# Performance work log

Measured on AMD Instinct MI355X. Metric: run time of the kernel, lower is better.

## Reference

```python
import jax, jax.numpy as jnp
import numpy as np

K_V = 0.5      # input voltage scaling
G_OFF = 1e-5   # off conductance (S)
G_ON = 1e-3    # on conductance (S)


def setup_inputs() -> dict:
    key = jax.random.key(0)
    k1, k2 = jax.random.split(key)
    batch, size_in, size_out = 256, 1024, 1024
    stdv = 1.0 / np.sqrt(size_in)
    x = jax.random.normal(k1, (batch, size_in), dtype=jnp.float32)
    weights = jax.random.normal(k2, (size_out, size_in), dtype=jnp.float32) * stdv
    bias = jnp.zeros((size_out,), dtype=jnp.float32)
    return {"x": x, "weights": weights, "bias": bias}


def reference(x, weights, bias):
    batch = x.shape[0]
    # append bias column of ones: inputs [batch, in+1]
    inputs = jnp.concatenate([x, jnp.ones((batch, 1), dtype=x.dtype)], axis=1)
    # weights_and_bias [in+1, out]
    wb = jnp.concatenate([weights.T, bias[None, :]], axis=0)
    V = K_V * inputs
    max_wb = jnp.max(jnp.abs(wb))
    k_G = (G_ON - G_OFF) / max_wb
    k_I = K_V * k_G
    G_eff = k_G * wb
    G_pos = G_OFF + jnp.maximum(G_eff, 0.0)
    G_neg = G_OFF - jnp.minimum(G_eff, 0.0)
    # interleave pos/neg columns -> G [in+1, 2*out]
    G = jnp.reshape(jnp.stack([G_pos, G_neg], axis=-1), (wb.shape[0], -1))
    # sum over input lines == matmul (avoids torch's [batch,in+1,2*out] intermediate)
    I = jnp.einsum('bi,io->bo', V, G)
    I_total = I[:, 0::2] - I[:, 1::2]
    return I_total / k_I
```

## Files before the change

kernel.cpp:

```cpp
#include <hip/hip_runtime.h>
#include <hip/hip_bf16.h>


typedef __attribute__((ext_vector_type(4))) float  f32x4;
typedef __attribute__((ext_vector_type(8))) short  bf16x8;

#define BATCH    256
#define SIZE_IN  1024
#define SIZE_OUT 1024

#define BM  64
#define BN  64
#define BK  64
#define LDK 72
#define NT  (SIZE_IN / BK)

__global__ __launch_bounds__(256)
void memristor_gemm(const float* __restrict__ X, const float* __restrict__ W,
                    const float* __restrict__ bias, float* __restrict__ out) {
    __shared__ alignas(16) ushort Alds[2][BM][LDK];
    __shared__ alignas(16) ushort Blds[2][BN][LDK];

    const int t    = threadIdx.x;
    const int lr   = t >> 4;
    const int lc   = (t & 15) << 2;
    const int brow = blockIdx.y * BM;
    const int bcol = blockIdx.x * BN;

    const int wid  = t >> 6;
    const int lane = t & 63;
    const int wr   = wid >> 1;
    const int wc   = wid & 1;
    const int fr   = lane & 15;
    const int fg   = lane >> 4;

    const float* Aptr = X + (size_t)(brow + lr) * SIZE_IN + lc;
    const float* Bptr = W + (size_t)(bcol + lr) * SIZE_IN + lc;

    f32x4 ar[4], br[4];

    auto stage = [&](int buf) {
        #pragma unroll
        for (int q = 0; q < 4; ++q) {
            union { struct { __hip_bfloat162 a, b; } h; uint2 u; } pa, pb;
            float2 f0; f0.x = ar[q].x; f0.y = ar[q].y;
            float2 f1; f1.x = ar[q].z; f1.y = ar[q].w;
            pa.h.a = __float22bfloat162_rn(f0);
            pa.h.b = __float22bfloat162_rn(f1);
            float2 g0; g0.x = br[q].x; g0.y = br[q].y;
            float2 g1; g1.x = br[q].z; g1.y = br[q].w;
            pb.h.a = __float22bfloat162_rn(g0);
            pb.h.b = __float22bfloat162_rn(g1);
            *(uint2*)&Alds[buf][lr + q * 16][lc] = pa.u;
            *(uint2*)&Blds[buf][lr + q * 16][lc] = pb.u;
        }
    };

    #pragma unroll
    for (int q = 0; q < 4; ++q) {
        ar[q] = *(const f32x4*)(Aptr + q * 16 * SIZE_IN);
        br[q] = *(const f32x4*)(Bptr + q * 16 * SIZE_IN);
    }
    stage(0);
    __syncthreads();

    const f32x4 zero = {0.f, 0.f, 0.f, 0.f};
    f32x4 acc[2][2] = {{zero, zero}, {zero, zero}};

    int cur = 0;
    for (int kt = 0; kt < NT; ++kt) {
        const bool pf = (kt + 1 < NT);
        if (pf) {
            const int k = (kt + 1) * BK;
            #pragma unroll
            for (int q = 0; q < 4; ++q) {
                ar[q] = *(const f32x4*)(Aptr + q * 16 * SIZE_IN + k);
                br[q] = *(const f32x4*)(Bptr + q * 16 * SIZE_IN + k);
            }
        }
        #pragma unroll
        for (int kk = 0; kk < 2; ++kk) {
            bf16x8 af[2], bfv[2];
            #pragma unroll
            for (int m = 0; m < 2; ++m)
                af[m] = *(const bf16x8*)&Alds[cur][wr * 32 + m * 16 + fr][kk * 32 + fg * 8];
            #pragma unroll
            for (int n = 0; n < 2; ++n)
                bfv[n] = *(const bf16x8*)&Blds[cur][wc * 32 + n * 16 + fr][kk * 32 + fg * 8];
            #pragma unroll
            for (int m = 0; m < 2; ++m)
                #pragma unroll
                for (int n = 0; n < 2; ++n)
                    acc[m][n] = __builtin_amdgcn_mfma_f32_16x16x32_bf16(
                        af[m], bfv[n], acc[m][n], 0, 0, 0);
        }
        if (pf) stage(cur ^ 1);
        __syncthreads();
        cur ^= 1;
    }

    #pragma unroll
    for (int n = 0; n < 2; ++n) {
        const int col = bcol + wc * 32 + n * 16 + fr;
        const float bv = bias[col];
        #pragma unroll
        for (int m = 0; m < 2; ++m) {
            const int row0 = brow + wr * 32 + m * 16 + fg * 4;
            #pragma unroll
            for (int j = 0; j < 4; ++j) {
                out[(size_t)(row0 + j) * SIZE_OUT + col] = acc[m][n][j] + bv;
            }
        }
    }
}

extern "C" void kernel_launch(void* const* d_in, const int* in_sizes, int n_in,
                              void* d_out, int out_size, void* d_ws, size_t ws_size,
                              hipStream_t stream) {
    const float* x  = (const float*)d_in[0];
    const float* w  = (const float*)d_in[1];
    const float* b  = (const float*)d_in[2];
    float* out      = (float*)d_out;

    dim3 grid(SIZE_OUT / BN, BATCH / BM);
    dim3 block(256);
    hipLaunchKernelGGL(memristor_gemm, grid, block, 0, stream, x, w, b, out);
}
```

Measured before the change: 73.02 us.

## Replace LDS-staged GEMM with register-direct MFMA loads and split-K reduction

```diff
diff --git a/kernel.cpp b/kernel.cpp
--- a/kernel.cpp
+++ b/kernel.cpp
@@ -9,108 +9,58 @@
 #define SIZE_IN  1024
 #define SIZE_OUT 1024
 
-#define BM  64
-#define BN  64
-#define BK  64
-#define LDK 72
-#define NT  (SIZE_IN / BK)
+static __device__ inline bf16x8 pack8(f32x4 lo, f32x4 hi) {
+    union { struct { __hip_bfloat162 a, b, c, d; } h; bf16x8 v; } u;
+    float2 f;
+    f.x = lo.x; f.y = lo.y; u.h.a = __float22bfloat162_rn(f);
+    f.x = lo.z; f.y = lo.w; u.h.b = __float22bfloat162_rn(f);
+    f.x = hi.x; f.y = hi.y; u.h.c = __float22bfloat162_rn(f);
+    f.x = hi.z; f.y = hi.w; u.h.d = __float22bfloat162_rn(f);
+    return u.v;
+}
 
-__global__ __launch_bounds__(256)
+__global__ __launch_bounds__(512, 2)
 void memristor_gemm(const float* __restrict__ X, const float* __restrict__ W,
                     const float* __restrict__ bias, float* __restrict__ out) {
-    __shared__ alignas(16) ushort Alds[2][BM][LDK];
-    __shared__ alignas(16) ushort Blds[2][BN][LDK];
+    __shared__ f32x4 red[4][64];
 
     const int t    = threadIdx.x;
-    const int lr   = t >> 4;
-    const int lc   = (t & 15) << 2;
-    const int brow = blockIdx.y * BM;
-    const int bcol = blockIdx.x * BN;
-
+    const int lane = t & 63;
     const int wid  = t >> 6;
-    const int lane = t & 63;
-    const int wr   = wid >> 1;
-    const int wc   = wid & 1;
+    const int ks   = wid >> 2;
+    const int wq   = wid & 3;
+    const int wr   = wq >> 1;
+    const int wc   = wq & 1;
     const int fr   = lane & 15;
     const int fg   = lane >> 4;
 
-    const float* Aptr = X + (size_t)(brow + lr) * SIZE_IN + lc;
-    const float* Bptr = W + (size_t)(bcol + lr) * SIZE_IN + lc;
+    const int brow = blockIdx.y * 32;
+    const int bcol = blockIdx.x * 32;
 
-    f32x4 ar[4], br[4];
+    const float* Ap = X + (size_t)(brow + wr * 16 + fr) * SIZE_IN + ks * 512 + fg * 8;
+    const float* Bp = W + (size_t)(bcol + wc * 16 + fr) * SIZE_IN + ks * 512 + fg * 8;
 
-    auto stage = [&](int buf) {
-        #pragma unroll
-        for (int q = 0; q < 4; ++q) {
-            union { struct { __hip_bfloat162 a, b; } h; uint2 u; } pa, pb;
-            float2 f0; f0.x = ar[q].x; f0.y = ar[q].y;
-            float2 f1; f1.x = ar[q].z; f1.y = ar[q].w;
-            pa.h.a = __float22bfloat162_rn(f0);
-            pa.h.b = __float22bfloat162_rn(f1);
-            float2 g0; g0.x = br[q].x; g0.y = br[q].y;
-            float2 g1; g1.x = br[q].z; g1.y = br[q].w;
-            pb.h.a = __float22bfloat162_rn(g0);
-            pb.h.b = __float22bfloat162_rn(g1);
-            *(uint2*)&Alds[buf][lr + q * 16][lc] = pa.u;
-            *(uint2*)&Blds[buf][lr + q * 16][lc] = pb.u;
-        }
-    };
-
+    f32x4 acc = {0.f, 0.f, 0.f, 0.f};
     #pragma unroll
-    for (int q = 0; q < 4; ++q) {
-        ar[q] = *(const f32x4*)(Aptr + q * 16 * SIZE_IN);
-        br[q] = *(const f32x4*)(Bptr + q * 16 * SIZE_IN);
-    }
-    stage(0);
-    __syncthreads();
-
-    const f32x4 zero = {0.f, 0.f, 0.f, 0.f};
-    f32x4 acc[2][2] = {{zero, zero}, {zero, zero}};
-
-    int cur = 0;
-    for (int kt = 0; kt < NT; ++kt) {
-        const bool pf = (kt + 1 < NT);
-        if (pf) {
-            const int k = (kt + 1) * BK;
-            #pragma unroll
-            for (int q = 0; q < 4; ++q) {
-                ar[q] = *(const f32x4*)(Aptr + q * 16 * SIZE_IN + k);
-                br[q] = *(const f32x4*)(Bptr + q * 16 * SIZE_IN + k);
-            }
-        }
-        #pragma unroll
-        for (int kk = 0; kk < 2; ++kk) {
-            bf16x8 af[2], bfv[2];
-            #pragma unroll
-            for (int m = 0; m < 2; ++m)
-                af[m] = *(const bf16x8*)&Alds[cur][wr * 32 + m * 16 + fr][kk * 32 + fg * 8];
-            #pragma unroll
-            for (int n = 0; n < 2; ++n)
-                bfv[n] = *(const bf16x8*)&Blds[cur][wc * 32 + n * 16 + fr][kk * 32 + fg * 8];
-            #pragma unroll
-            for (int m = 0; m < 2; ++m)
-                #pragma unroll
-                for (int n = 0; n < 2; ++n)
-                    acc[m][n] = __builtin_amdgcn_mfma_f32_16x16x32_bf16(
-                        af[m], bfv[n], acc[m][n], 0, 0, 0);
-        }
-        if (pf) stage(cur ^ 1);
-        __syncthreads();
-        cur ^= 1;
+    for (int kk = 0; kk < 16; ++kk) {
+        f32x4 a0 = *(const f32x4*)(Ap + kk * 32);
+        f32x4 a1 = *(const f32x4*)(Ap + kk * 32 + 4);
+        f32x4 b0 = *(const f32x4*)(Bp + kk * 32);
+        f32x4 b1 = *(const f32x4*)(Bp + kk * 32 + 4);
+        acc = __builtin_amdgcn_mfma_f32_16x16x32_bf16(pack8(a0, a1), pack8(b0, b1),
+                                                      acc, 0, 0, 0);
     }
 
-    #pragma unroll
-    for (int n = 0; n < 2; ++n) {
-        const int col = bcol + wc * 32 + n * 16 + fr;
-        const float bv = bias[col];
+    if (ks == 1) red[wq][lane] = acc;
+    __syncthreads();
+    if (ks == 0) {
+        const f32x4 other = red[wq][lane];
+        const int col    = bcol + wc * 16 + fr;
+        const float bv   = bias[col];
+        const int row0   = brow + wr * 16 + fg * 4;
         #pragma unroll
-        for (int m = 0; m < 2; ++m) {
-            const int row0 = brow + wr * 32 + m * 16 + fg * 4;
-            #pragma unroll
-            for (int j = 0; j < 4; ++j) {
-                out[(size_t)(row0 + j) * SIZE_OUT + col] = acc[m][n][j] + bv;
-            }
-        }
+        for (int j = 0; j < 4; ++j)
+            out[(size_t)(row0 + j) * SIZE_OUT + col] = acc[j] + other[j] + bv;
     }
 }
 
@@ -122,7 +72,7 @@
     const float* b  = (const float*)d_in[2];
     float* out      = (float*)d_out;
 
-    dim3 grid(SIZE_OUT / BN, BATCH / BM);
-    dim3 block(256);
+    dim3 grid(SIZE_OUT / 32, BATCH / 32);
+    dim3 block(512);
     hipLaunchKernelGGL(memristor_gemm, grid, block, 0, stream, x, w, b, out);
 }
```

Result: no change. 73.69 us (+0.9%).
